# Performance work log

Hardware: AMD Instinct MI355X
Metric: run time of the kernel (lower is better)

Reference implementation:

```python
import jax, jax.numpy as jnp
import numpy as np

EMB_DIM = 128
HIDDEN = 1024
CL_TEMPERATURE = 0.5
NUM_LABELS = 20
EPS = 1e-14


def setup_inputs() -> dict:
    key = jax.random.key(0)
    k1, k2, k3, k4, k5, k6 = jax.random.split(key, 6)
    B, L = 4, 128
    token_repr = jax.random.normal(k1, (B, L, HIDDEN), dtype=jnp.float32)
    labels = jax.random.randint(k2, (B, L), 0, NUM_LABELS, dtype=jnp.int64)
    mask = jnp.ones((B, L), dtype=jnp.int64)
    # Linear params (PyTorch default init scale ~ U(-1/sqrt(fan_in), 1/sqrt(fan_in)))
    s = 1.0 / np.sqrt(HIDDEN)
    W_mu = jax.random.uniform(k3, (HIDDEN, EMB_DIM), jnp.float32, -s, s)
    b_mu = jax.random.uniform(k4, (EMB_DIM,), jnp.float32, -s, s)
    W_sigma = jax.random.uniform(k5, (HIDDEN, EMB_DIM), jnp.float32, -s, s)
    b_sigma = jax.random.uniform(k6, (EMB_DIM,), jnp.float32, -s, s)
    return {"token_repr": token_repr, "labels": labels, "mask": mask,
            "W_mu": W_mu, "b_mu": b_mu, "W_sigma": W_sigma, "b_sigma": b_sigma}


def _pairwise_sym_kl(mu, sigma):
    """Symmetric diagonal-Gaussian KL between all pairs. mu,sigma: [N,D] -> [N,N]."""
    D = mu.shape[-1]
    mu_i, mu_j = mu[:, None, :], mu[None, :, :]          # [N,N,D] broadcast
    si, sj = sigma[:, None, :], sigma[None, :, :]
    r_ij = sj / si                                        # [N,N,D]
    ij_kl = 0.5 * (r_ij.sum(-1)
                   + (((mu_i - mu_j) ** 2) / si).sum(-1)
                   - D
                   - jnp.log(r_ij + EPS).sum(-1))
    r_ji = si / sj
    ji_kl = 0.5 * (r_ji.sum(-1)
                   + (((mu_j - mu_i) ** 2) / sj).sum(-1)
                   - D
                   - jnp.log(r_ji + EPS).sum(-1))
    return 0.5 * (ij_kl + ji_kl)


def reference(token_repr, labels, mask, W_mu, b_mu, W_sigma, b_sigma):
    h = jax.nn.relu(token_repr)                           # nn.ReLU before Linear
    mu = (h @ W_mu + b_mu).reshape(-1, EMB_DIM)           # [N,D]
    sigma = (jax.nn.elu(h @ W_sigma + b_sigma) + 1.0 + EPS).reshape(-1, EMB_DIM)
    lab = labels.reshape(-1)
    valid = (mask.reshape(-1) == 1) & (lab > 0)           # torch does this by filtering; we mask

    # loss = -symmetric KL for all pairs (cl_type='kl')
    loss = -_pairwise_sym_kl(mu, sigma)                   # [N,N]

    # denominator mask: all embedding dims differ (excludes self / duplicates)
    all_diff = jnp.all(mu[:, None, :] != mu[None, :, :], axis=-1)
    den_mask = all_diff & valid[:, None] & valid[None, :]
    num_mask = den_mask & (lab[:, None] == lab[None, :])

    # NT-Xent with masked reduction; rows with zero positives (or invalid) dropped
    e = jnp.exp(loss / CL_TEMPERATURE)                    # kl >= 0 so e <= 1, stable
    cnts = jnp.sum(num_mask, axis=1).astype(loss.dtype)
    loss_num = jnp.sum(e * num_mask, axis=1)
    loss_den = jnp.sum(e * den_mask, axis=1)
    include = cnts > 0
    safe = lambda x: jnp.where(include, x, 1.0)
    loss_final = -jnp.log(safe(loss_num)) + jnp.log(safe(loss_den)) + jnp.log(safe(cnts))
    n_inc = jnp.maximum(jnp.sum(include), 1).astype(loss.dtype)
    return jnp.sum(jnp.where(include, loss_final, 0.0)) / n_inc
```

## Files before the change

### kernel.cpp

```cpp
#include <hip/hip_runtime.h>
#include <math.h>

#define N_TOK 512
#define DIM   128
#define KDIM  1024
#define EPSF  1e-14f

__global__ __launch_bounds__(512) void proj_fused(
    const float* __restrict__ token, const float* __restrict__ Wmu,
    const float* __restrict__ bmu, const float* __restrict__ Wsg,
    const float* __restrict__ bsg, float* __restrict__ mu,
    float* __restrict__ sg, float* __restrict__ iv)
{
    __shared__ float hs[8][KDIM];
    __shared__ float4 red[3][8][16];
    const int bid = blockIdx.x;
    const int t = threadIdx.x;

    const int rowg = bid >> 2, colsel = bid & 3;
    const int m = colsel >> 1, ch = colsel & 1;

    {
        const float4* src = (const float4*)(token + (size_t)rowg * 8 * KDIM);
        float4* dst = (float4*)&hs[0][0];
        #pragma unroll
        for (int r = 0; r < 4; ++r) {
            int idx = t + r * 512;
            float4 v = src[idx];
            v.x = fmaxf(v.x, 0.f); v.y = fmaxf(v.y, 0.f);
            v.z = fmaxf(v.z, 0.f); v.w = fmaxf(v.w, 0.f);
            dst[idx] = v;
        }
    }
    __syncthreads();

    const int q = t & 15, rsub = t >> 4;
    const int row = rsub & 7, kq = rsub >> 3;
    const int d = ch * 64 + q * 4;
    const float* __restrict__ W = (m ? Wsg : Wmu) + (size_t)(kq * 256) * DIM + d;
    const float4* hp = (const float4*)(&hs[row][kq * 256]);

    float4 acc = make_float4(0.f, 0.f, 0.f, 0.f);
    #pragma unroll 4
    for (int k4 = 0; k4 < 64; ++k4) {
        float4 h = hp[k4];
        const float* wp = W + (size_t)(k4 * 4) * DIM;
        float4 w0 = *(const float4*)(wp);
        float4 w1 = *(const float4*)(wp + DIM);
        float4 w2 = *(const float4*)(wp + 2 * DIM);
        float4 w3 = *(const float4*)(wp + 3 * DIM);
        acc.x = fmaf(h.x, w0.x, acc.x); acc.y = fmaf(h.x, w0.y, acc.y);
        acc.z = fmaf(h.x, w0.z, acc.z); acc.w = fmaf(h.x, w0.w, acc.w);
        acc.x = fmaf(h.y, w1.x, acc.x); acc.y = fmaf(h.y, w1.y, acc.y);
        acc.z = fmaf(h.y, w1.z, acc.z); acc.w = fmaf(h.y, w1.w, acc.w);
        acc.x = fmaf(h.z, w2.x, acc.x); acc.y = fmaf(h.z, w2.y, acc.y);
        acc.z = fmaf(h.z, w2.z, acc.z); acc.w = fmaf(h.z, w2.w, acc.w);
        acc.x = fmaf(h.w, w3.x, acc.x); acc.y = fmaf(h.w, w3.y, acc.y);
        acc.z = fmaf(h.w, w3.z, acc.z); acc.w = fmaf(h.w, w3.w, acc.w);
    }

    if (kq > 0) red[kq - 1][row][q] = acc;
    __syncthreads();
    if (kq == 0) {
        float4 r0 = red[0][row][q], r1 = red[1][row][q], r2 = red[2][row][q];
        acc.x += r0.x + r1.x + r2.x; acc.y += r0.y + r1.y + r2.y;
        acc.z += r0.z + r1.z + r2.z; acc.w += r0.w + r1.w + r2.w;
        const int rowi = rowg * 8 + row;
        if (m == 0) {
            float4 b = *(const float4*)(bmu + d);
            acc.x += b.x; acc.y += b.y; acc.z += b.z; acc.w += b.w;
            *(float4*)(mu + (size_t)rowi * DIM + d) = acc;
        } else {
            float4 b = *(const float4*)(bsg + d);
            float x0 = acc.x + b.x, x1 = acc.y + b.y;
            float x2 = acc.z + b.z, x3 = acc.w + b.w;
            float4 e, vv;
            e.x = (x0 > 0.f ? x0 : expm1f(x0)) + 1.0f + EPSF;
            e.y = (x1 > 0.f ? x1 : expm1f(x1)) + 1.0f + EPSF;
            e.z = (x2 > 0.f ? x2 : expm1f(x2)) + 1.0f + EPSF;
            e.w = (x3 > 0.f ? x3 : expm1f(x3)) + 1.0f + EPSF;
            vv.x = 1.0f / e.x; vv.y = 1.0f / e.y;
            vv.z = 1.0f / e.z; vv.w = 1.0f / e.w;
            *(float4*)(sg + (size_t)rowi * DIM + d) = e;
            *(float4*)(iv + (size_t)rowi * DIM + d) = vv;
        }
    }
}

__global__ __launch_bounds__(256) void packT(
    const float* __restrict__ mu, const float* __restrict__ sg,
    const float* __restrict__ iv, float4* __restrict__ jpack)
{
    __shared__ float tmu[8][132], tsg[8][132], tiv[8][132];
    const int rg = blockIdx.x;
    const int t = threadIdx.x;
    const int q = t & 31, r = t >> 5;
    const int row = rg * 8 + r;
    const int d = q * 4;

    *(float4*)(&tmu[r][d]) = *(const float4*)(mu + (size_t)row * DIM + d);
    *(float4*)(&tsg[r][d]) = *(const float4*)(sg + (size_t)row * DIM + d);
    *(float4*)(&tiv[r][d]) = *(const float4*)(iv + (size_t)row * DIM + d);
    __syncthreads();

    const int dd = t >> 1, rr = (t & 1) * 4;
    #pragma unroll
    for (int k = 0; k < 4; ++k) {
        float4 o = make_float4(tmu[rr + k][dd], tsg[rr + k][dd], tiv[rr + k][dd], 0.f);
        jpack[(size_t)dd * N_TOK + rg * 8 + rr + k] = o;
    }
}

__global__ __launch_bounds__(256) void pair_kernel(
    const float* __restrict__ mu, const float* __restrict__ sg,
    const float* __restrict__ iv, const float4* __restrict__ jpack,
    const int* __restrict__ labels, const int* __restrict__ mask,
    float* __restrict__ gpart)
{
    __shared__ float si[3][16][DIM];
    __shared__ int slab[16], svalid[16];
    const int ig = blockIdx.x >> 4, jg = blockIdx.x & 15;
    const int i0 = ig * 16, j0 = jg * 32;
    const int t = threadIdx.x;

    #pragma unroll
    for (int rep = 0; rep < 2; ++rep) {
        int f = t + rep * 256;
        int row = f >> 5, kq = f & 31;
        size_t off = (size_t)(i0 + row) * DIM + kq * 4;
        ((float4*)&si[0][0][0])[f] = *(const float4*)(mu + off);
        ((float4*)&si[1][0][0])[f] = *(const float4*)(sg + off);
        ((float4*)&si[2][0][0])[f] = *(const float4*)(iv + off);
    }
    if (t < 16) {
        int lab = labels[i0 + t];
        slab[t] = lab;
        svalid[t] = (mask[i0 + t] == 1 && lab > 0) ? 1 : 0;
    }
    __syncthreads();

    const int jl = t & 31, isub = t >> 5;
    const int ia = 2 * isub, ib = ia + 1;
    const int j = j0 + jl;
    const int labj = labels[j];
    const bool validj = (mask[j] == 1) && (labj > 0);

    const float4* jp = jpack + j;

    float accA = 0.f, accB = 0.f;
    float mnA = 1e30f, mnB = 1e30f;

    #pragma unroll 4
    for (int q = 0; q < 32; ++q) {
        const int d0 = q * 4;
        float4 p0 = jp[(size_t)(d0 + 0) * N_TOK];
        float4 p1 = jp[(size_t)(d0 + 1) * N_TOK];
        float4 p2 = jp[(size_t)(d0 + 2) * N_TOK];
        float4 p3 = jp[(size_t)(d0 + 3) * N_TOK];

        float4 bmA = *(const float4*)(&si[0][ia][d0]);
        float4 bsA = *(const float4*)(&si[1][ia][d0]);
        float4 bvA = *(const float4*)(&si[2][ia][d0]);
        float4 bmB = *(const float4*)(&si[0][ib][d0]);
        float4 bsB = *(const float4*)(&si[1][ib][d0]);
        float4 bvB = *(const float4*)(&si[2][ib][d0]);

        float dm;
        dm = bmA.x - p0.x; accA = fmaf(fmaf(dm, dm, p0.y), bvA.x, fmaf(fmaf(dm, dm, bsA.x), p0.z, accA)); mnA = fminf(mnA, fabsf(dm));
        dm = bmA.y - p1.x; accA = fmaf(fmaf(dm, dm, p1.y), bvA.y, fmaf(fmaf(dm, dm, bsA.y), p1.z, accA)); mnA = fminf(mnA, fabsf(dm));
        dm = bmA.z - p2.x; accA = fmaf(fmaf(dm, dm, p2.y), bvA.z, fmaf(fmaf(dm, dm, bsA.z), p2.z, accA)); mnA = fminf(mnA, fabsf(dm));
        dm = bmA.w - p3.x; accA = fmaf(fmaf(dm, dm, p3.y), bvA.w, fmaf(fmaf(dm, dm, bsA.w), p3.z, accA)); mnA = fminf(mnA, fabsf(dm));

        dm = bmB.x - p0.x; accB = fmaf(fmaf(dm, dm, p0.y), bvB.x, fmaf(fmaf(dm, dm, bsB.x), p0.z, accB)); mnB = fminf(mnB, fabsf(dm));
        dm = bmB.y - p1.x; accB = fmaf(fmaf(dm, dm, p1.y), bvB.y, fmaf(fmaf(dm, dm, bsB.y), p1.z, accB)); mnB = fminf(mnB, fabsf(dm));
        dm = bmB.z - p2.x; accB = fmaf(fmaf(dm, dm, p2.y), bvB.z, fmaf(fmaf(dm, dm, bsB.z), p2.z, accB)); mnB = fminf(mnB, fabsf(dm));
        dm = bmB.w - p3.x; accB = fmaf(fmaf(dm, dm, p3.y), bvB.w, fmaf(fmaf(dm, dm, bsB.w), p3.z, accB)); mnB = fminf(mnB, fabsf(dm));
    }

    float eA = expf(128.0f - 0.5f * accA);
    float eB = expf(128.0f - 0.5f * accB);
    bool pvA = validj && (svalid[ia] != 0) && (mnA != 0.0f);
    bool pvB = validj && (svalid[ib] != 0) && (mnB != 0.0f);
    bool smA = pvA && (labj == slab[ia]);
    bool smB = pvB && (labj == slab[ib]);
    float dA = pvA ? eA : 0.f, nA = smA ? eA : 0.f, cA = smA ? 1.f : 0.f;
    float dB = pvB ? eB : 0.f, nB = smB ? eB : 0.f, cB = smB ? 1.f : 0.f;

    #pragma unroll
    for (int m = 1; m < 32; m <<= 1) {
        cA += __shfl_xor(cA, m); nA += __shfl_xor(nA, m); dA += __shfl_xor(dA, m);
        cB += __shfl_xor(cB, m); nB += __shfl_xor(nB, m); dB += __shfl_xor(dB, m);
    }
    if (jl == 0) {
        float* pa = gpart + ((size_t)jg * N_TOK + i0 + ia) * 3;
        float* pb = gpart + ((size_t)jg * N_TOK + i0 + ib) * 3;
        pa[0] = cA; pa[1] = nA; pa[2] = dA;
        pb[0] = cB; pb[1] = nB; pb[2] = dB;
    }
}

__global__ __launch_bounds__(512) void final_kernel(
    const float* __restrict__ gpart, float* __restrict__ out)
{
    __shared__ float redL[8], redI[8];
    const int t = threadIdx.x;
    float c = 0.f, nm = 0.f, dn = 0.f;
    #pragma unroll
    for (int jg = 0; jg < 16; ++jg) {
        const float* p = gpart + ((size_t)jg * N_TOK + t) * 3;
        c += p[0]; nm += p[1]; dn += p[2];
    }
    const bool inc = c > 0.5f;
    float lf = inc ? (-logf(nm) + logf(dn) + logf(c)) : 0.f;
    float fi = inc ? 1.f : 0.f;
    #pragma unroll
    for (int m = 1; m < 64; m <<= 1) {
        lf += __shfl_xor(lf, m);
        fi += __shfl_xor(fi, m);
    }
    if ((t & 63) == 0) { redL[t >> 6] = lf; redI[t >> 6] = fi; }
    __syncthreads();
    if (t == 0) {
        float L = 0.f, I = 0.f;
        #pragma unroll
        for (int w = 0; w < 8; ++w) { L += redL[w]; I += redI[w]; }
        out[0] = L / fmaxf(I, 1.0f);
    }
}

extern "C" void kernel_launch(void* const* d_in, const int* in_sizes, int n_in,
                              void* d_out, int out_size, void* d_ws, size_t ws_size,
                              hipStream_t stream) {
    const float* token  = (const float*)d_in[0];
    const int*   labels = (const int*)d_in[1];
    const int*   mask   = (const int*)d_in[2];
    const float* Wmu    = (const float*)d_in[3];
    const float* bmu    = (const float*)d_in[4];
    const float* Wsg    = (const float*)d_in[5];
    const float* bsg    = (const float*)d_in[6];

    float* ws = (float*)d_ws;
    float*  mu    = ws;
    float*  sg    = mu + 65536;
    float*  iv    = sg + 65536;
    float4* jpack = (float4*)(iv + 65536);
    float*  gpart = (float*)(jpack + 65536);

    proj_fused<<<256, 512, 0, stream>>>(token, Wmu, bmu, Wsg, bsg, mu, sg, iv);
    packT<<<64, 256, 0, stream>>>(mu, sg, iv, jpack);
    pair_kernel<<<512, 256, 0, stream>>>(mu, sg, iv, jpack, labels, mask, gpart);
    final_kernel<<<1, 512, 0, stream>>>(gpart, (float*)d_out);
}
```

Baseline: 106.5 us.

## Fuse transposed j-layout writes into projection and drop packT kernel

The projection kernel now writes transposed copies of mu (as float) and sigma/inverse-sigma (as float2) directly, which removes the separate packT transpose kernel and one launch. The pair kernel reads these two split arrays instead of a padded float4 pack, so per-element j traffic drops from 16 to 12 bytes. In exchange the transposed stores from the projection are strided scalar and float2 writes that coalesce poorly, and the pair loop issues two loads per dimension instead of one.

```diff
diff --git a/kernel.cpp b/kernel.cpp
--- a/kernel.cpp
+++ b/kernel.cpp
@@ -6,11 +6,12 @@
 #define KDIM  1024
 #define EPSF  1e-14f
 
-__global__ __launch_bounds__(512) void proj_fused(
+__global__ __launch_bounds__(512) void projT(
     const float* __restrict__ token, const float* __restrict__ Wmu,
     const float* __restrict__ bmu, const float* __restrict__ Wsg,
     const float* __restrict__ bsg, float* __restrict__ mu,
-    float* __restrict__ sg, float* __restrict__ iv)
+    float* __restrict__ sg, float* __restrict__ iv,
+    float* __restrict__ jmuT, float2* __restrict__ jsviT)
 {
     __shared__ float hs[8][KDIM];
     __shared__ float4 red[3][8][16];
@@ -70,6 +71,10 @@
             float4 b = *(const float4*)(bmu + d);
             acc.x += b.x; acc.y += b.y; acc.z += b.z; acc.w += b.w;
             *(float4*)(mu + (size_t)rowi * DIM + d) = acc;
+            jmuT[(size_t)(d + 0) * N_TOK + rowi] = acc.x;
+            jmuT[(size_t)(d + 1) * N_TOK + rowi] = acc.y;
+            jmuT[(size_t)(d + 2) * N_TOK + rowi] = acc.z;
+            jmuT[(size_t)(d + 3) * N_TOK + rowi] = acc.w;
         } else {
             float4 b = *(const float4*)(bsg + d);
             float x0 = acc.x + b.x, x1 = acc.y + b.y;
@@ -83,39 +88,19 @@
             vv.z = 1.0f / e.z; vv.w = 1.0f / e.w;
             *(float4*)(sg + (size_t)rowi * DIM + d) = e;
             *(float4*)(iv + (size_t)rowi * DIM + d) = vv;
+            jsviT[(size_t)(d + 0) * N_TOK + rowi] = make_float2(e.x, vv.x);
+            jsviT[(size_t)(d + 1) * N_TOK + rowi] = make_float2(e.y, vv.y);
+            jsviT[(size_t)(d + 2) * N_TOK + rowi] = make_float2(e.z, vv.z);
+            jsviT[(size_t)(d + 3) * N_TOK + rowi] = make_float2(e.w, vv.w);
         }
-    }
-}
-
-__global__ __launch_bounds__(256) void packT(
-    const float* __restrict__ mu, const float* __restrict__ sg,
-    const float* __restrict__ iv, float4* __restrict__ jpack)
-{
-    __shared__ float tmu[8][132], tsg[8][132], tiv[8][132];
-    const int rg = blockIdx.x;
-    const int t = threadIdx.x;
-    const int q = t & 31, r = t >> 5;
-    const int row = rg * 8 + r;
-    const int d = q * 4;
-
-    *(float4*)(&tmu[r][d]) = *(const float4*)(mu + (size_t)row * DIM + d);
-    *(float4*)(&tsg[r][d]) = *(const float4*)(sg + (size_t)row * DIM + d);
-    *(float4*)(&tiv[r][d]) = *(const float4*)(iv + (size_t)row * DIM + d);
-    __syncthreads();
-
-    const int dd = t >> 1, rr = (t & 1) * 4;
-    #pragma unroll
-    for (int k = 0; k < 4; ++k) {
-        float4 o = make_float4(tmu[rr + k][dd], tsg[rr + k][dd], tiv[rr + k][dd], 0.f);
-        jpack[(size_t)dd * N_TOK + rg * 8 + rr + k] = o;
     }
 }
 
 __global__ __launch_bounds__(256) void pair_kernel(
     const float* __restrict__ mu, const float* __restrict__ sg,
-    const float* __restrict__ iv, const float4* __restrict__ jpack,
-    const int* __restrict__ labels, const int* __restrict__ mask,
-    float* __restrict__ gpart)
+    const float* __restrict__ iv, const float* __restrict__ jmuT,
+    const float2* __restrict__ jsviT, const int* __restrict__ labels,
+    const int* __restrict__ mask, float* __restrict__ gpart)
 {
     __shared__ float si[3][16][DIM];
     __shared__ int slab[16], svalid[16];
@@ -145,7 +130,8 @@
     const int labj = labels[j];
     const bool validj = (mask[j] == 1) && (labj > 0);
 
-    const float4* jp = jpack + j;
+    const float*  pmT = jmuT  + j;
+    const float2* psT = jsviT + j;
 
     float accA = 0.f, accB = 0.f;
     float mnA = 1e30f, mnB = 1e30f;
@@ -153,10 +139,14 @@
     #pragma unroll 4
     for (int q = 0; q < 32; ++q) {
         const int d0 = q * 4;
-        float4 p0 = jp[(size_t)(d0 + 0) * N_TOK];
-        float4 p1 = jp[(size_t)(d0 + 1) * N_TOK];
-        float4 p2 = jp[(size_t)(d0 + 2) * N_TOK];
-        float4 p3 = jp[(size_t)(d0 + 3) * N_TOK];
+        float  jm0 = pmT[(size_t)(d0 + 0) * N_TOK];
+        float  jm1 = pmT[(size_t)(d0 + 1) * N_TOK];
+        float  jm2 = pmT[(size_t)(d0 + 2) * N_TOK];
+        float  jm3 = pmT[(size_t)(d0 + 3) * N_TOK];
+        float2 sv0 = psT[(size_t)(d0 + 0) * N_TOK];
+        float2 sv1 = psT[(size_t)(d0 + 1) * N_TOK];
+        float2 sv2 = psT[(size_t)(d0 + 2) * N_TOK];
+        float2 sv3 = psT[(size_t)(d0 + 3) * N_TOK];
 
         float4 bmA = *(const float4*)(&si[0][ia][d0]);
         float4 bsA = *(const float4*)(&si[1][ia][d0]);
@@ -166,15 +156,15 @@
         float4 bvB = *(const float4*)(&si[2][ib][d0]);
 
         float dm;
-        dm = bmA.x - p0.x; accA = fmaf(fmaf(dm, dm, p0.y), bvA.x, fmaf(fmaf(dm, dm, bsA.x), p0.z, accA)); mnA = fminf(mnA, fabsf(dm));
-        dm = bmA.y - p1.x; accA = fmaf(fmaf(dm, dm, p1.y), bvA.y, fmaf(fmaf(dm, dm, bsA.y), p1.z, accA)); mnA = fminf(mnA, fabsf(dm));
-        dm = bmA.z - p2.x; accA = fmaf(fmaf(dm, dm, p2.y), bvA.z, fmaf(fmaf(dm, dm, bsA.z), p2.z, accA)); mnA = fminf(mnA, fabsf(dm));
-        dm = bmA.w - p3.x; accA = fmaf(fmaf(dm, dm, p3.y), bvA.w, fmaf(fmaf(dm, dm, bsA.w), p3.z, accA)); mnA = fminf(mnA, fabsf(dm));
-
-        dm = bmB.x - p0.x; accB = fmaf(fmaf(dm, dm, p0.y), bvB.x, fmaf(fmaf(dm, dm, bsB.x), p0.z, accB)); mnB = fminf(mnB, fabsf(dm));
-        dm = bmB.y - p1.x; accB = fmaf(fmaf(dm, dm, p1.y), bvB.y, fmaf(fmaf(dm, dm, bsB.y), p1.z, accB)); mnB = fminf(mnB, fabsf(dm));
-        dm = bmB.z - p2.x; accB = fmaf(fmaf(dm, dm, p2.y), bvB.z, fmaf(fmaf(dm, dm, bsB.z), p2.z, accB)); mnB = fminf(mnB, fabsf(dm));
-        dm = bmB.w - p3.x; accB = fmaf(fmaf(dm, dm, p3.y), bvB.w, fmaf(fmaf(dm, dm, bsB.w), p3.z, accB)); mnB = fminf(mnB, fabsf(dm));
+        dm = bmA.x - jm0; accA = fmaf(fmaf(dm, dm, sv0.x), bvA.x, fmaf(fmaf(dm, dm, bsA.x), sv0.y, accA)); mnA = fminf(mnA, fabsf(dm));
+        dm = bmA.y - jm1; accA = fmaf(fmaf(dm, dm, sv1.x), bvA.y, fmaf(fmaf(dm, dm, bsA.y), sv1.y, accA)); mnA = fminf(mnA, fabsf(dm));
+        dm = bmA.z - jm2; accA = fmaf(fmaf(dm, dm, sv2.x), bvA.z, fmaf(fmaf(dm, dm, bsA.z), sv2.y, accA)); mnA = fminf(mnA, fabsf(dm));
+        dm = bmA.w - jm3; accA = fmaf(fmaf(dm, dm, sv3.x), bvA.w, fmaf(fmaf(dm, dm, bsA.w), sv3.y, accA)); mnA = fminf(mnA, fabsf(dm));
+
+        dm = bmB.x - jm0; accB = fmaf(fmaf(dm, dm, sv0.x), bvB.x, fmaf(fmaf(dm, dm, bsB.x), sv0.y, accB)); mnB = fminf(mnB, fabsf(dm));
+        dm = bmB.y - jm1; accB = fmaf(fmaf(dm, dm, sv1.x), bvB.y, fmaf(fmaf(dm, dm, bsB.y), sv1.y, accB)); mnB = fminf(mnB, fabsf(dm));
+        dm = bmB.z - jm2; accB = fmaf(fmaf(dm, dm, sv2.x), bvB.z, fmaf(fmaf(dm, dm, bsB.z), sv2.y, accB)); mnB = fminf(mnB, fabsf(dm));
+        dm = bmB.w - jm3; accB = fmaf(fmaf(dm, dm, sv3.x), bvB.w, fmaf(fmaf(dm, dm, bsB.w), sv3.y, accB)); mnB = fminf(mnB, fabsf(dm));
     }
 
     float eA = expf(128.0f - 0.5f * accA);
@@ -239,15 +229,17 @@
     const float* Wsg    = (const float*)d_in[5];
     const float* bsg    = (const float*)d_in[6];
 
-    float* ws = (float*)d_ws;
+    float*  ws    = (float*)d_ws;
     float*  mu    = ws;
     float*  sg    = mu + 65536;
     float*  iv    = sg + 65536;
-    float4* jpack = (float4*)(iv + 65536);
-    float*  gpart = (float*)(jpack + 65536);
-
-    proj_fused<<<256, 512, 0, stream>>>(token, Wmu, bmu, Wsg, bsg, mu, sg, iv);
-    packT<<<64, 256, 0, stream>>>(mu, sg, iv, jpack);
-    pair_kernel<<<512, 256, 0, stream>>>(mu, sg, iv, jpack, labels, mask, gpart);
+    float*  jmuT  = iv + 65536;
+    float2* jsviT = (float2*)(jmuT + 65536);
+    float*  gpart = (float*)(jsviT + 65536);
+
+    projT<<<256, 512, 0, stream>>>(token, Wmu, bmu, Wsg, bsg, mu, sg, iv,
+                                   jmuT, jsviT);
+    pair_kernel<<<512, 256, 0, stream>>>(mu, sg, iv, jmuT, jsviT, labels, mask,
+                                         gpart);
     final_kernel<<<1, 512, 0, stream>>>(gpart, (float*)d_out);
 }
```

Result: no change. 105.5 us (-0.9%).
